# Optimization experiments

Measured on AMD Instinct MI355X. Metric: run time of the kernel, lower is better.

The kernel has to match this reference:

```python
import jax, jax.numpy as jnp
import numpy as np

B, IN_C, N, K, KS, OUT_C = 8, 64, 4096, 20, 20, 64
FEATS = 2 * IN_C  # conv expects in_c*2 channels; view requires feats*KS/K == 2*in_c
BN_EPS = 1e-5


def setup_inputs() -> dict:
    key = jax.random.key(0)
    k1, k2, k3, k4, k5 = jax.random.split(key, 5)
    feature = jax.random.normal(k1, (B, FEATS, N), dtype=jnp.float32)
    permatrix = jax.random.normal(k2, (B * N, K, KS), dtype=jnp.float32)
    conv_w = jax.random.normal(k3, (OUT_C, FEATS), dtype=jnp.float32)  # 1x1 Conv2d weight squeezed
    conv_b = jax.random.normal(k4, (OUT_C,), dtype=jnp.float32)
    bn_gamma = jnp.ones((OUT_C,), dtype=jnp.float32)
    bn_beta = jnp.zeros((OUT_C,), dtype=jnp.float32)
    spirals_index = jax.random.randint(k5, (B * N * K,), 0, B * N, dtype=jnp.int64)
    return {"feature": feature, "permatrix": permatrix, "conv_w": conv_w,
            "conv_b": conv_b, "bn_gamma": bn_gamma, "bn_beta": bn_beta,
            "spirals_index": spirals_index}


def reference(feature, permatrix, conv_w, conv_b, bn_gamma, bn_beta, spirals_index):
    bsize, feats, num_pts = feature.shape
    # [B, C, N] -> [B*N, C]
    flat = feature.transpose(0, 2, 1).reshape(bsize * num_pts, feats)
    # gather k spiral neighbors per point: [B*N, K, C] -> [B*N, C, K]
    spirals = flat[spirals_index].reshape(bsize * num_pts, K, feats).transpose(0, 2, 1)
    # per-point batched matmul with learned permutation matrix: [B*N, C, KS]
    spirals = jnp.einsum('pck,pks->pcs', spirals, permatrix)
    # faithful torch .view(B, N, K, -1) memory reinterpretation (C-order reshape)
    feat = spirals.reshape(bsize, num_pts, K, -1)          # [B, N, K, 2*in_c]
    x = feat.transpose(0, 3, 1, 2)                          # [B, 2*in_c, N, K]
    # 1x1 conv == channel GEMM
    y = jnp.einsum('oc,bcnk->bonk', conv_w, x) + conv_b[None, :, None, None]
    # max over neighbor dim -> [B, out_c, N]
    y = jnp.max(y, axis=-1)
    # BatchNorm1d (training mode: batch statistics over (B, N), biased var)
    mean = jnp.mean(y, axis=(0, 2), keepdims=True)
    var = jnp.mean((y - mean) ** 2, axis=(0, 2), keepdims=True)
    out = (y - mean) * jax.lax.rsqrt(var + BN_EPS)
    out = out * bn_gamma[None, :, None] + bn_beta[None, :, None]
    return out
```

## Files before the change

### kernel.cpp

```cpp
#include <hip/hip_runtime.h>
#include <hip/hip_bf16.h>

typedef short short8 __attribute__((ext_vector_type(8)));
typedef short short4v __attribute__((ext_vector_type(4)));
typedef float f32x4 __attribute__((ext_vector_type(4)));
typedef unsigned int uint2v __attribute__((ext_vector_type(2)));

#define NPTS 4096
#define BATCH 8
#define PTOT 32768
#define FEATS 128
#define KK 20
#define OUTC 64
#define PTS_PER_WAVE 8
#define WAVES 4

__device__ __forceinline__ unsigned short f2bf(float f){
  union { __hip_bfloat16 h; unsigned short u; } v;
  v.h = __hip_bfloat16(f);
  return v.u;
}

__device__ __forceinline__ void gload_lds16(const void* src, void* dst){
  __builtin_amdgcn_global_load_lds((const __attribute__((address_space(1))) void*)src,
                                   (__attribute__((address_space(3))) void*)dst, 16, 0, 0);
}

__global__ void k_transpose(const float* __restrict__ f, unsigned short* __restrict__ flat){
  __shared__ float tile[32][33];
  int b = blockIdx.z, c0 = blockIdx.y*32, n0 = blockIdx.x*32;
  int tx = threadIdx.x, ty = threadIdx.y;
  const float* src = f + ((size_t)b*FEATS + c0)*NPTS + n0;
  #pragma unroll
  for(int i=0;i<4;i++) tile[ty+8*i][tx] = src[(size_t)(ty+8*i)*NPTS + tx];
  __syncthreads();
  unsigned short* dst = flat + ((size_t)b*NPTS + n0)*FEATS + c0;
  #pragma unroll
  for(int i=0;i<4;i++) dst[(size_t)(ty+8*i)*FEATS + tx] = f2bf(tile[tx][ty+8*i]);
}

__global__ void k_wpack(const float* __restrict__ convw, unsigned short* __restrict__ wp){
  int e = blockIdx.x*256 + threadIdx.x;
  int j = e & 7, l15 = (e>>3)&15, lg = (e>>7)&3, n2 = (e>>9)&3, ks = e>>11;
  int o = n2*16 + l15, c = ks*32 + lg*8 + j;
  wp[e] = f2bf(convw[o*FEATS + c]);
}

__global__ __launch_bounds__(256, 3) void k_main(
    const unsigned short* __restrict__ flat,
    const float* __restrict__ perm_g,
    const unsigned short* __restrict__ wpack,
    const int*   __restrict__ idx_g,
    float* __restrict__ out,
    float* __restrict__ stats)
{
  const int t = threadIdx.x, lane = t & 63, w = t >> 6;
  const int l15 = lane & 15, lg = lane >> 4;

  __shared__ __align__(16) unsigned short gbuf_all[WAVES][2560];
  __shared__ __align__(16) unsigned short tbuf_all[WAVES][2560];
  __shared__ __align__(16) float pbuf_all[WAVES][2][400];
  __shared__ __align__(16) unsigned short W_lds[8192];
  __shared__ int   idx_all[WAVES][160];
  __shared__ float ybuf_all[WAVES][4*OUTC];

  unsigned short* gbuf = gbuf_all[w];
  unsigned short* tbuf = tbuf_all[w];
  int*   idxb = idx_all[w];
  float* ybuf = ybuf_all[w];
  const unsigned gbufb = (unsigned)(size_t)(const __attribute__((address_space(3))) void*)gbuf;

  const int p0 = blockIdx.x*(WAVES*PTS_PER_WAVE) + w*PTS_PER_WAVE;

  {
    const int* ib = idx_g + (size_t)p0*KK;
    idxb[lane]      = ib[lane];
    idxb[64+lane]   = ib[64+lane];
    if(lane < 32) idxb[128+lane] = ib[128+lane];
  }

  #pragma unroll
  for(int it=0; it<4; it++){
    gload_lds16((const char*)wpack + it*4096 + (size_t)t*16,
                (char*)W_lds + it*4096 + w*1024);
  }
  asm volatile("s_waitcnt vmcnt(0)" ::: "memory");
  __syncthreads();

  int krowb4[5], colb[5];
  #pragma unroll
  for(int it=0; it<5; it++){
    int q = it*64 + lane;
    int cg = q/40, r = q - cg*40;
    int kgr = r>>3, rem = r&7, krem = rem>>1, chalf = rem&1;
    krowb4[it] = (kgr*4 + krem)*4;
    colb[it]   = cg*32 + chalf*16;
  }

  int kg0 = 2*lg;   if(kg0 > 4) kg0 = 0;
  int kg1 = 2*lg+1; if(kg1 > 4) kg1 = 0;
  const unsigned tra0 = gbufb + kg0*128 + l15*8;
  const unsigned tra1 = gbufb + kg1*128 + l15*8;

  const int s2 = (l15 < 4) ? (16 + l15) : 19;
  int koff[8];
  #pragma unroll
  for(int j=0;j<8;j++){ int kb = lg*160 + j*20; koff[j] = (kb > 380) ? 380 : kb; }

  float bsum[4] = {0,0,0,0}, bsq[4] = {0,0,0,0};

  #define STAGE_G(PI) do{                                                       \
    int pib_ = (PI)*80;                                                         \
    _Pragma("unroll")                                                           \
    for(int it_=0; it_<5; it_++){                                               \
      int id_ = *(const int*)((const char*)idxb + pib_ + krowb4[it_]);          \
      const char* s_ = (const char*)flat + ((size_t)(unsigned)id_*256) + colb[it_]; \
      gload_lds16(s_, (char*)gbuf + it_*1024);                                  \
    } }while(0)

  #define STAGE_P(PI) do{                                                       \
    const char* ps_ = (const char*)(perm_g + (size_t)(p0+(PI))*400);            \
    char* pd_ = (char*)&pbuf_all[w][(PI)&1][0];                                 \
    gload_lds16(ps_ + (size_t)lane*16, pd_);                                    \
    gload_lds16(ps_ + 576 + (size_t)lane*16, pd_ + 576);                        \
  }while(0)

  STAGE_G(0); STAGE_P(0); STAGE_P(1);

  const int bb = p0 >> 12, nn0 = p0 & (NPTS-1);

  for(int pi=0; pi<PTS_PER_WAVE; pi++){
    if(pi == PTS_PER_WAVE-1) asm volatile("s_waitcnt vmcnt(0)" ::: "memory");
    else                     asm volatile("s_waitcnt vmcnt(2)" ::: "memory");

    if(pi == 4){
      float* op = out + ((size_t)bb*OUTC + lane)*NPTS + nn0;
      float4 v;
      v.x = ybuf[0*64+lane]; v.y = ybuf[1*64+lane];
      v.z = ybuf[2*64+lane]; v.w = ybuf[3*64+lane];
      *(float4*)op = v;
    }

    short4v lo[8], hi[8];
    #pragma unroll
    for(int nt=0; nt<8; nt++){
      asm volatile("ds_read_b64_tr_b16 %0, %1 offset:%2" : "=v"(lo[nt]) : "v"(tra0), "i"(nt*640));
      asm volatile("ds_read_b64_tr_b16 %0, %1 offset:%2" : "=v"(hi[nt]) : "v"(tra1), "i"(nt*640));
    }
    const float* pb = &pbuf_all[w][pi&1][0];
    float p0r[8], p1r[8];
    #pragma unroll
    for(int j=0;j<8;j++){ p0r[j] = pb[koff[j]+l15]; p1r[j] = pb[koff[j]+s2]; }

    asm volatile("s_waitcnt lgkmcnt(0)" ::: "memory");
    __builtin_amdgcn_sched_barrier(0);

    if(pi+1 < PTS_PER_WAVE) STAGE_G(pi+1);
    if(pi+2 < PTS_PER_WAVE) STAGE_P(pi+2);

    short8 a0f, a1f;
    #pragma unroll
    for(int j=0;j<8;j++){
      int kk2 = lg*8 + j;
      a0f[j] = (kk2 < KK) ? (short)f2bf(p0r[j]) : (short)0;
      a1f[j] = (kk2 < KK) ? (short)f2bf(p1r[j]) : (short)0;
    }

    #pragma unroll
    for(int nt=0; nt<8; nt++){
      short8 gf = __builtin_shufflevector(lo[nt], hi[nt], 0,1,2,3,4,5,6,7);
      f32x4 z = {0.f,0.f,0.f,0.f};
      f32x4 c0 = __builtin_amdgcn_mfma_f32_16x16x32_bf16(a0f, gf, z, 0,0,0);
      f32x4 c1 = __builtin_amdgcn_mfma_f32_16x16x32_bf16(a1f, gf, z, 0,0,0);
      const int c = nt*16 + l15;
      {
        int f0 = c*20 + lg*4;
        int byt = (f0*2) ^ (((f0>>7)&7)<<4);
        uint2v pk;
        pk.x = (unsigned)f2bf(c0[0]) | ((unsigned)f2bf(c0[1])<<16);
        pk.y = (unsigned)f2bf(c0[2]) | ((unsigned)f2bf(c0[3])<<16);
        *(uint2v*)((char*)tbuf + byt) = pk;
      }
      if(lg == 0){
        int f0 = c*20 + 16;
        int byt = (f0*2) ^ (((f0>>7)&7)<<4);
        uint2v pk;
        pk.x = (unsigned)f2bf(c1[0]) | ((unsigned)f2bf(c1[1])<<16);
        pk.y = (unsigned)f2bf(c1[2]) | ((unsigned)f2bf(c1[3])<<16);
        *(uint2v*)((char*)tbuf + byt) = pk;
      }
    }

    f32x4 acc[2][4];
    #pragma unroll
    for(int m2=0;m2<2;m2++)
      #pragma unroll
      for(int n2=0;n2<4;n2++){ f32x4 z={0.f,0.f,0.f,0.f}; acc[m2][n2]=z; }

    const int kp1 = (l15 < 4) ? (16 + l15) : 19;
    #pragma unroll
    for(int ks=0; ks<4; ks++){
      int a0b = (l15*256 + ks*64 + lg*16) ^ ((l15&7)<<4);
      int a1b = (kp1*256 + ks*64 + lg*16) ^ ((kp1&7)<<4);
      short8 t0 = *(const short8*)((const char*)tbuf + a0b);
      short8 t1 = *(const short8*)((const char*)tbuf + a1b);
      #pragma unroll
      for(int n2=0; n2<4; n2++){
        short8 wf = *(const short8*)((const char*)W_lds + (ks*4+n2)*1024 + lane*16);
        acc[0][n2] = __builtin_amdgcn_mfma_f32_16x16x32_bf16(t0, wf, acc[0][n2], 0,0,0);
        acc[1][n2] = __builtin_amdgcn_mfma_f32_16x16x32_bf16(t1, wf, acc[1][n2], 0,0,0);
      }
    }

    #pragma unroll
    for(int n2=0; n2<4; n2++){
      float m0 = fmaxf(fmaxf(acc[0][n2][0], acc[0][n2][1]),
                       fmaxf(acc[0][n2][2], acc[0][n2][3]));
      float m1 = fmaxf(fmaxf(acc[1][n2][0], acc[1][n2][1]),
                       fmaxf(acc[1][n2][2], acc[1][n2][3]));
      float mm = fmaxf(m0, (lg == 0) ? m1 : -3.4e38f);
      mm = fmaxf(mm, __shfl_xor(mm, 16));
      mm = fmaxf(mm, __shfl_xor(mm, 32));
      if(lg == 0) ybuf[(pi&3)*64 + n2*16 + l15] = mm;
      bsum[n2] += mm; bsq[n2] += mm*mm;
    }
  }

  {
    float* op = out + ((size_t)bb*OUTC + lane)*NPTS + nn0 + 4;
    float4 v;
    v.x = ybuf[0*64+lane]; v.y = ybuf[1*64+lane];
    v.z = ybuf[2*64+lane]; v.w = ybuf[3*64+lane];
    *(float4*)op = v;
  }

  float* red = (float*)&idx_all[0][0];
  __syncthreads();
  if(lg == 0){
    #pragma unroll
    for(int n2=0; n2<4; n2++){
      int o = n2*16 + l15;
      red[w*128 + o]      = bsum[n2];
      red[w*128 + 64 + o] = bsq[n2];
    }
  }
  __syncthreads();
  if(w == 0){
    float s = red[lane] + red[128+lane] + red[256+lane] + red[384+lane];
    atomicAdd(&stats[lane], s);
  } else if(w == 1){
    float s = red[64+lane] + red[192+lane] + red[320+lane] + red[448+lane];
    atomicAdd(&stats[64+lane], s);
  }
}

__global__ void k_bn2(float* __restrict__ out, const float* __restrict__ stats,
                      const float* __restrict__ gamma, const float* __restrict__ beta){
  __shared__ float ss[128];
  int t = threadIdx.x;
  if(t < 64){
    float inv = 1.f/(float)PTOT;
    float mean = stats[t]*inv;
    float var  = stats[64+t]*inv - mean*mean;
    float rstd = rsqrtf(var + 1e-5f);
    float sc = gamma[t]*rstd;
    ss[t]    = sc;
    ss[64+t] = beta[t] - mean*sc;
  }
  __syncthreads();
  int i = blockIdx.x*256 + t;
  float4 v = ((float4*)out)[i];
  int o = (i >> 10) & 63;
  float sc = ss[o], sh = ss[64+o];
  v.x = v.x*sc + sh; v.y = v.y*sc + sh; v.z = v.z*sc + sh; v.w = v.w*sc + sh;
  ((float4*)out)[i] = v;
}

extern "C" void kernel_launch(void* const* d_in, const int* in_sizes, int n_in,
                              void* d_out, int out_size, void* d_ws, size_t ws_size,
                              hipStream_t stream){
  (void)in_sizes; (void)n_in; (void)ws_size;
  const float* feature    = (const float*)d_in[0];
  const float* permatrix  = (const float*)d_in[1];
  const float* conv_w     = (const float*)d_in[2];
  const float* bn_gamma   = (const float*)d_in[4];
  const float* bn_beta    = (const float*)d_in[5];
  const int*   sp_idx     = (const int*)d_in[6];
  float* out = (float*)d_out;

  unsigned short* flat  = (unsigned short*)d_ws;
  float* stats          = (float*)((char*)d_ws + (size_t)8*1024*1024);
  unsigned short* wpack = (unsigned short*)((char*)d_ws + (size_t)8*1024*1024 + 4096);

  hipMemsetAsync(stats, 0, 128*sizeof(float), stream);

  dim3 gT(NPTS/32, FEATS/32, BATCH), bT(32,8);
  k_transpose<<<gT, bT, 0, stream>>>(feature, flat);
  k_wpack<<<dim3(32), dim3(256), 0, stream>>>(conv_w, wpack);

  k_main<<<dim3(PTOT/(WAVES*PTS_PER_WAVE)), dim3(256), 0, stream>>>(
      flat, permatrix, wpack, sp_idx, out, stats);

  k_bn2<<<dim3(out_size/4/256), dim3(256), 0, stream>>>(out, stats, bn_gamma, bn_beta);
}
```

Before: 81.50 us.

## Alias gather and transposed buffers in LDS and shrink output staging

The per-wave gather buffer and the transposed intermediate buffer now share one LDS region. To make this safe, the next point's gather prefetch is issued only after the second GEMM has read the transposed data. The y staging buffer shrinks from four points to two, so output is written as float2 every two points instead of float4 every four. The aim is to cut LDS use per block so more blocks fit per CU, at the cost of a shorter prefetch lead before each gather is consumed and narrower global stores.

```diff
diff --git a/kernel.cpp b/kernel.cpp
--- a/kernel.cpp
+++ b/kernel.cpp
@@ -57,18 +57,16 @@
   const int t = threadIdx.x, lane = t & 63, w = t >> 6;
   const int l15 = lane & 15, lg = lane >> 4;
 
-  __shared__ __align__(16) unsigned short gbuf_all[WAVES][2560];
-  __shared__ __align__(16) unsigned short tbuf_all[WAVES][2560];
+  __shared__ __align__(16) unsigned short buf_all[WAVES][2560];
   __shared__ __align__(16) float pbuf_all[WAVES][2][400];
   __shared__ __align__(16) unsigned short W_lds[8192];
   __shared__ int   idx_all[WAVES][160];
-  __shared__ float ybuf_all[WAVES][4*OUTC];
-
-  unsigned short* gbuf = gbuf_all[w];
-  unsigned short* tbuf = tbuf_all[w];
+  __shared__ float ybuf_all[WAVES][2*OUTC];
+
+  unsigned short* buf = buf_all[w];
   int*   idxb = idx_all[w];
   float* ybuf = ybuf_all[w];
-  const unsigned gbufb = (unsigned)(size_t)(const __attribute__((address_space(3))) void*)gbuf;
+  const unsigned bufb = (unsigned)(size_t)(const __attribute__((address_space(3))) void*)buf;
 
   const int p0 = blockIdx.x*(WAVES*PTS_PER_WAVE) + w*PTS_PER_WAVE;
 
@@ -99,8 +97,8 @@
 
   int kg0 = 2*lg;   if(kg0 > 4) kg0 = 0;
   int kg1 = 2*lg+1; if(kg1 > 4) kg1 = 0;
-  const unsigned tra0 = gbufb + kg0*128 + l15*8;
-  const unsigned tra1 = gbufb + kg1*128 + l15*8;
+  const unsigned tra0 = bufb + kg0*128 + l15*8;
+  const unsigned tra1 = bufb + kg1*128 + l15*8;
 
   const int s2 = (l15 < 4) ? (16 + l15) : 19;
   int koff[8];
@@ -115,7 +113,7 @@
     for(int it_=0; it_<5; it_++){                                               \
       int id_ = *(const int*)((const char*)idxb + pib_ + krowb4[it_]);          \
       const char* s_ = (const char*)flat + ((size_t)(unsigned)id_*256) + colb[it_]; \
-      gload_lds16(s_, (char*)gbuf + it_*1024);                                  \
+      gload_lds16(s_, (char*)buf + it_*1024);                                   \
     } }while(0)
 
   #define STAGE_P(PI) do{                                                       \
@@ -133,12 +131,12 @@
     if(pi == PTS_PER_WAVE-1) asm volatile("s_waitcnt vmcnt(0)" ::: "memory");
     else                     asm volatile("s_waitcnt vmcnt(2)" ::: "memory");
 
-    if(pi == 4){
-      float* op = out + ((size_t)bb*OUTC + lane)*NPTS + nn0;
-      float4 v;
-      v.x = ybuf[0*64+lane]; v.y = ybuf[1*64+lane];
-      v.z = ybuf[2*64+lane]; v.w = ybuf[3*64+lane];
-      *(float4*)op = v;
+    if(pi >= 2 && (pi & 1) == 0){
+      float* op = out + ((size_t)bb*OUTC + lane)*NPTS + nn0 + (pi-2);
+      float2 v;
+      v.x = ybuf[lane];
+      v.y = ybuf[64 + lane];
+      *(float2*)op = v;
     }
 
     short4v lo[8], hi[8];
@@ -154,9 +152,6 @@
 
     asm volatile("s_waitcnt lgkmcnt(0)" ::: "memory");
     __builtin_amdgcn_sched_barrier(0);
-
-    if(pi+1 < PTS_PER_WAVE) STAGE_G(pi+1);
-    if(pi+2 < PTS_PER_WAVE) STAGE_P(pi+2);
 
     short8 a0f, a1f;
     #pragma unroll
@@ -179,7 +174,7 @@
         uint2v pk;
         pk.x = (unsigned)f2bf(c0[0]) | ((unsigned)f2bf(c0[1])<<16);
         pk.y = (unsigned)f2bf(c0[2]) | ((unsigned)f2bf(c0[3])<<16);
-        *(uint2v*)((char*)tbuf + byt) = pk;
+        *(uint2v*)((char*)buf + byt) = pk;
       }
       if(lg == 0){
         int f0 = c*20 + 16;
@@ -187,7 +182,7 @@
         uint2v pk;
         pk.x = (unsigned)f2bf(c1[0]) | ((unsigned)f2bf(c1[1])<<16);
         pk.y = (unsigned)f2bf(c1[2]) | ((unsigned)f2bf(c1[3])<<16);
-        *(uint2v*)((char*)tbuf + byt) = pk;
+        *(uint2v*)((char*)buf + byt) = pk;
       }
     }
 
@@ -202,8 +197,8 @@
     for(int ks=0; ks<4; ks++){
       int a0b = (l15*256 + ks*64 + lg*16) ^ ((l15&7)<<4);
       int a1b = (kp1*256 + ks*64 + lg*16) ^ ((kp1&7)<<4);
-      short8 t0 = *(const short8*)((const char*)tbuf + a0b);
-      short8 t1 = *(const short8*)((const char*)tbuf + a1b);
+      short8 t0 = *(const short8*)((const char*)buf + a0b);
+      short8 t1 = *(const short8*)((const char*)buf + a1b);
       #pragma unroll
       for(int n2=0; n2<4; n2++){
         short8 wf = *(const short8*)((const char*)W_lds + (ks*4+n2)*1024 + lane*16);
@@ -211,6 +206,9 @@
         acc[1][n2] = __builtin_amdgcn_mfma_f32_16x16x32_bf16(t1, wf, acc[1][n2], 0,0,0);
       }
     }
+
+    if(pi+1 < PTS_PER_WAVE) STAGE_G(pi+1);
+    if(pi+2 < PTS_PER_WAVE) STAGE_P(pi+2);
 
     #pragma unroll
     for(int n2=0; n2<4; n2++){
@@ -221,17 +219,17 @@
       float mm = fmaxf(m0, (lg == 0) ? m1 : -3.4e38f);
       mm = fmaxf(mm, __shfl_xor(mm, 16));
       mm = fmaxf(mm, __shfl_xor(mm, 32));
-      if(lg == 0) ybuf[(pi&3)*64 + n2*16 + l15] = mm;
+      if(lg == 0) ybuf[(pi&1)*64 + n2*16 + l15] = mm;
       bsum[n2] += mm; bsq[n2] += mm*mm;
     }
   }
 
   {
-    float* op = out + ((size_t)bb*OUTC + lane)*NPTS + nn0 + 4;
-    float4 v;
-    v.x = ybuf[0*64+lane]; v.y = ybuf[1*64+lane];
-    v.z = ybuf[2*64+lane]; v.w = ybuf[3*64+lane];
-    *(float4*)op = v;
+    float* op = out + ((size_t)bb*OUTC + lane)*NPTS + nn0 + 6;
+    float2 v;
+    v.x = ybuf[lane];
+    v.y = ybuf[64 + lane];
+    *(float2*)op = v;
   }
 
   float* red = (float*)&idx_all[0][0];
```

After: 83.12 us. About the same (+2.0%).
